# Performance work log

Measured on AMD Instinct MI355X. Metric: run time of the kernel, lower is better.

## Reference

```python
import jax, jax.numpy as jnp
import numpy as np

SEQ, D_IN, D_OUT = 8192, 768, 768

def setup_inputs() -> dict:
    key = jax.random.key(0)
    k1, k2, k3, k4 = jax.random.split(key, 4)
    scale = 1.0 / np.sqrt(D_IN)
    return {
        "x": jax.random.normal(k1, (SEQ, D_IN), dtype=jnp.float32),
        "w_q": jax.random.normal(k2, (D_OUT, D_IN), dtype=jnp.float32) * scale,
        "w_k": jax.random.normal(k3, (D_OUT, D_IN), dtype=jnp.float32) * scale,
        "w_v": jax.random.normal(k4, (D_OUT, D_IN), dtype=jnp.float32) * scale,
    }

def reference(x, w_q, w_k, w_v):
    # torch Linear: y = x @ W.T (no bias since qkv_bias=False)
    q = x @ w_q.T  # [S, D]
    k = x @ w_k.T  # [S, D]
    v = x @ w_v.T  # [S, D]
    scores = (q @ k.T) / jnp.sqrt(jnp.asarray(k.shape[-1], x.dtype))  # [S, S]
    attn = jax.nn.softmax(scores, axis=-1)
    return attn @ v  # [S, D]
```

## Files before the change

### kernel.cpp

```cpp
#include <hip/hip_runtime.h>

#define SEQ 8192
#define DIM 768

typedef __attribute__((ext_vector_type(8))) short s16x8;
typedef __attribute__((ext_vector_type(4))) float f32x4;

__device__ __forceinline__ unsigned short f2bf(float f) {
  union { float f; unsigned u; } v; v.f = f;
  unsigned r = v.u + 0x7FFFu + ((v.u >> 16) & 1u);
  return (unsigned short)(r >> 16);
}

__device__ __forceinline__ float bf2f(unsigned short s) {
  union { unsigned u; float f; } v; v.u = ((unsigned)s) << 16;
  return v.f;
}

__device__ __forceinline__ void gll16(const void* gsrc, void* ldst) {
  __builtin_amdgcn_global_load_lds(
      (__attribute__((address_space(1))) unsigned int*)gsrc,
      (__attribute__((address_space(3))) unsigned int*)ldst, 16, 0, 0);
}

#define XN4 (SEQ * DIM / 4)
#define WN4 (DIM * DIM / 4)

__global__ void cast_all_kernel(const float* __restrict__ x, const float* __restrict__ wq,
                                const float* __restrict__ wk, const float* __restrict__ wv,
                                unsigned short* __restrict__ dx, unsigned short* __restrict__ dq,
                                unsigned short* __restrict__ dk, unsigned short* __restrict__ dv) {
  int i = blockIdx.x * blockDim.x + threadIdx.x;
  const float* s;
  unsigned short* d;
  int off;
  if (i < XN4) {
    s = x; d = dx; off = i;
  } else {
    int j = i - XN4;
    int wi = j / WN4;
    off = j - wi * WN4;
    s = (wi == 0) ? wq : ((wi == 1) ? wk : wv);
    d = (wi == 0) ? dq : ((wi == 1) ? dk : dv);
  }
  float4 v = ((const float4*)s)[off];
  ushort4 r; r.x = f2bf(v.x); r.y = f2bf(v.y); r.z = f2bf(v.z); r.w = f2bf(v.w);
  ((ushort4*)d)[off] = r;
}

__global__ __launch_bounds__(256, 2)
void proj_kernel(const unsigned short* __restrict__ X,
                 const unsigned short* __restrict__ Wq,
                 const unsigned short* __restrict__ Wk,
                 const unsigned short* __restrict__ Wv,
                 unsigned short* __restrict__ Qb,
                 unsigned short* __restrict__ Kb,
                 unsigned short* __restrict__ Vtb) {
  __shared__ __align__(16) char lds[65536];
  const int tid = threadIdx.x;
  const int lane = tid & 63, wv = tid >> 6;
  const int l15 = lane & 15, l4 = lane >> 4;
  const int mt = blockIdx.x, nt = blockIdx.y, z = blockIdx.z;
  const unsigned short* W = (z == 0) ? Wq : ((z == 1) ? Wk : Wv);

  f32x4 acc[4][4];
#pragma unroll
  for (int i = 0; i < 4; ++i)
#pragma unroll
    for (int j = 0; j < 4; ++j) acc[i][j] = f32x4{0.f, 0.f, 0.f, 0.f};

  auto stage = [&](int kk) {
    char* At = lds + (kk & 1) * 32768;
    char* Bt = At + 16384;
    const int d0 = kk * 64;
#pragma unroll
    for (int i = 0; i < 4; ++i) {
      int s = i * 256 + tid;
      int row = s >> 3, c = (s & 7) ^ (row & 7);
      gll16(X + (long)(mt * 128 + row) * DIM + d0 + c * 8, At + i * 4096 + (wv << 10));
      gll16(W + (long)(nt * 128 + row) * DIM + d0 + c * 8, Bt + i * 4096 + (wv << 10));
    }
  };

  stage(0);
#pragma unroll 1
  for (int kk = 0; kk < 12; ++kk) {
    __syncthreads();
    if (kk + 1 < 12) stage(kk + 1);
    const char* At = lds + (kk & 1) * 32768;
    const char* Bt = At + 16384;
#pragma unroll
    for (int ks = 0; ks < 2; ++ks) {
      const int c = ks * 4 + l4;
      s16x8 a[4], b[4];
#pragma unroll
      for (int mi = 0; mi < 4; ++mi) {
        int row = (wv & 1) * 64 + mi * 16 + l15;
        a[mi] = *(const s16x8*)(At + row * 128 + ((c ^ (row & 7)) << 4));
      }
#pragma unroll
      for (int ni = 0; ni < 4; ++ni) {
        int row = (wv >> 1) * 64 + ni * 16 + l15;
        b[ni] = *(const s16x8*)(Bt + row * 128 + ((c ^ (row & 7)) << 4));
      }
#pragma unroll
      for (int mi = 0; mi < 4; ++mi)
#pragma unroll
        for (int ni = 0; ni < 4; ++ni)
          acc[mi][ni] = __builtin_amdgcn_mfma_f32_16x16x32_bf16(a[mi], b[ni], acc[mi][ni], 0, 0, 0);
    }
  }

#pragma unroll
  for (int mi = 0; mi < 4; ++mi)
#pragma unroll
    for (int ni = 0; ni < 4; ++ni) {
      int row0 = mt * 128 + (wv & 1) * 64 + mi * 16 + l4 * 4;
      int col = nt * 128 + (wv >> 1) * 64 + ni * 16 + l15;
      if (z == 2) {
        ushort4 r;
        r.x = f2bf(acc[mi][ni][0]); r.y = f2bf(acc[mi][ni][1]);
        r.z = f2bf(acc[mi][ni][2]); r.w = f2bf(acc[mi][ni][3]);
        *(ushort4*)(Vtb + (long)(row0 >> 5) * (DIM * 32) + col * 32 + (row0 & 31)) = r;
      } else {
        unsigned short* dst = (z == 0) ? Qb : Kb;
#pragma unroll
        for (int g = 0; g < 4; ++g)
          dst[(long)(row0 + g) * DIM + col] = f2bf(acc[mi][ni][g]);
      }
    }
}

#define SCALE_LOG2E 0.05205878f

#define LOADVB(arr, vv)                                                            \
  do {                                                                             \
    const unsigned short* Vb_ = V + (long)(kblk0 + (vv)) * (DIM * 32);             \
    _Pragma("unroll")                                                              \
    for (int j_ = 0; j_ < 6; ++j_)                                                 \
      arr[j_] = *(const s16x8*)(Vb_ + (j_ * 128 + wv * 16 + l15) * 32 + l4 * 8);   \
  } while (0)

#define PVCHUNK(vv, CUR, NXT)                                                      \
  do {                                                                             \
    if ((vv) + 1 < 8) LOADVB(NXT, (vv) + 1);                                       \
    s16x8 pa_[4];                                                                  \
    const int ck_ = (vv) * 4 + l4;                                                 \
    _Pragma("unroll")                                                              \
    for (int rs_ = 0; rs_ < 4; ++rs_) {                                            \
      int row_ = rs_ * 16 + l15;                                                   \
      int pc_ = (ck_ & ~7) | ((ck_ & 7) ^ (row_ & 7));                             \
      pa_[rs_] = *(const s16x8*)(Pl + row_ * 512 + (pc_ << 4));                    \
    }                                                                              \
    __builtin_amdgcn_s_setprio(1);                                                 \
    _Pragma("unroll")                                                              \
    for (int j_ = 0; j_ < 6; ++j_)                                                 \
      _Pragma("unroll")                                                            \
      for (int rs_ = 0; rs_ < 4; ++rs_)                                            \
        acc_o[rs_][j_] =                                                           \
            __builtin_amdgcn_mfma_f32_16x16x32_bf16(pa_[rs_], CUR[j_], acc_o[rs_][j_], 0, 0, 0); \
    __builtin_amdgcn_s_setprio(0);                                                 \
  } while (0)

__global__ __launch_bounds__(512, 2)
void flash_kernel(const unsigned short* __restrict__ Q,
                  const unsigned short* __restrict__ K,
                  const unsigned short* __restrict__ V,
                  unsigned short* __restrict__ partp,
                  float* __restrict__ outf,
                  float* __restrict__ lout,
                  int kv_len, int norm_out) {
  __shared__ __align__(16) char lds[114688];
  char* Pl = lds + 81920;
  float* l_part = (float*)lds;

  const int tid = threadIdx.x;
  const int lane = tid & 63, wv = tid >> 6;
  const int l15 = lane & 15, l4 = lane >> 4;
  const int qtile = blockIdx.x, split = blockIdx.y;
  const long kv0 = (long)split * kv_len;
  const long qrow0 = (long)qtile * 64;
  const int R = wv & 1;
  const int C = wv >> 1;

  f32x4 acc_o[4][6];
  float acc_lp[8];
#pragma unroll
  for (int i = 0; i < 4; ++i)
#pragma unroll
    for (int j = 0; j < 6; ++j) acc_o[i][j] = f32x4{0.f, 0.f, 0.f, 0.f};
#pragma unroll
  for (int i = 0; i < 8; ++i) acc_lp[i] = 0.f;

  const int niter = kv_len >> 8;

  auto stageQK = [&](int r, long kbase) {
    char* Qc = lds + (r & 1) * 40960;
    char* Kc = Qc + 8192;
    const int d0 = r * 64;
    {
      int s = tid;
      int row = s >> 3, c = (s & 7) ^ (row & 7);
      gll16(Q + (qrow0 + row) * DIM + d0 + c * 8, Qc + (wv << 10));
    }
#pragma unroll
    for (int i = 0; i < 4; ++i) {
      int s = i * 512 + tid;
      int row = s >> 3, c = (s & 7) ^ (row & 7);
      gll16(K + (kbase + row) * DIM + d0 + c * 8, Kc + i * 8192 + (wv << 10));
    }
  };

  stageQK(0, kv0);
#pragma unroll 1
  for (int it = 0; it < niter; ++it) {
    const long kb = kv0 + (long)it * 256;
    const long kblk0 = kb >> 5;

    f32x4 acc_s[2][4];
#pragma unroll
    for (int a = 0; a < 2; ++a)
#pragma unroll
      for (int b = 0; b < 4; ++b) acc_s[a][b] = f32x4{0.f, 0.f, 0.f, 0.f};

#pragma unroll 1
    for (int r = 0; r < 12; ++r) {
      __syncthreads();
      if (r + 1 < 12) stageQK(r + 1, kb);
      else if (it + 1 < niter) stageQK(0, kb + 256);
      const char* Qc = lds + (r & 1) * 40960;
      const char* Kc = Qc + 8192;
#pragma unroll
      for (int ks = 0; ks < 2; ++ks) {
        const int c = ks * 4 + l4;
        s16x8 af[2], bk[4];
#pragma unroll
        for (int rt = 0; rt < 2; ++rt) {
          int row = R * 32 + rt * 16 + l15;
          af[rt] = *(const s16x8*)(Qc + row * 128 + ((c ^ (row & 7)) << 4));
        }
#pragma unroll
        for (int ct = 0; ct < 4; ++ct) {
          int kr = C * 64 + ct * 16 + l15;
          bk[ct] = *(const s16x8*)(Kc + kr * 128 + ((c ^ (kr & 7)) << 4));
        }
        __builtin_amdgcn_s_setprio(1);
#pragma unroll
        for (int rt = 0; rt < 2; ++rt)
#pragma unroll
          for (int ct = 0; ct < 4; ++ct)
            acc_s[rt][ct] = __builtin_amdgcn_mfma_f32_16x16x32_bf16(af[rt], bk[ct], acc_s[rt][ct], 0, 0, 0);
        __builtin_amdgcn_s_setprio(0);
      }
    }

    s16x8 vbA[6], vbB[6];
    LOADVB(vbA, 0);

#pragma unroll
    for (int rt = 0; rt < 2; ++rt)
#pragma unroll
      for (int ct = 0; ct < 4; ++ct)
#pragma unroll
        for (int g = 0; g < 4; ++g) {
          float p = exp2f(acc_s[rt][ct][g] * SCALE_LOG2E);
          acc_lp[rt * 4 + g] += p;
          int row = R * 32 + rt * 16 + l4 * 4 + g;
          int col = C * 64 + ct * 16 + l15;
          int off = row * 512 + ((((col >> 3) ^ (row & 7))) << 4) + ((col & 7) << 1);
          *(unsigned short*)(Pl + off) = f2bf(p);
        }
    __syncthreads();

    PVCHUNK(0, vbA, vbB);
    PVCHUNK(1, vbB, vbA);
    PVCHUNK(2, vbA, vbB);
    PVCHUNK(3, vbB, vbA);
    PVCHUNK(4, vbA, vbB);
    PVCHUNK(5, vbB, vbA);
    PVCHUNK(6, vbA, vbB);
    PVCHUNK(7, vbB, vbA);
  }

#pragma unroll
  for (int i = 0; i < 8; ++i) {
    float v = acc_lp[i];
    v += __shfl_xor(v, 1); v += __shfl_xor(v, 2);
    v += __shfl_xor(v, 4); v += __shfl_xor(v, 8);
    acc_lp[i] = v;
  }
  __syncthreads();
  if (l15 == 0) {
#pragma unroll
    for (int rt = 0; rt < 2; ++rt)
#pragma unroll
      for (int g = 0; g < 4; ++g)
        l_part[C * 64 + R * 32 + rt * 16 + l4 * 4 + g] = acc_lp[rt * 4 + g];
  }
  __syncthreads();

  if (!norm_out) {
    if (tid < 64)
      lout[(long)split * SEQ + qrow0 + tid] =
          l_part[tid] + l_part[64 + tid] + l_part[128 + tid] + l_part[192 + tid];
#pragma unroll
    for (int rt = 0; rt < 4; ++rt) {
      int row = rt * 16 + l4 * 4;
#pragma unroll
      for (int j = 0; j < 6; ++j) {
        int cc = j >> 1, t = j & 1;
        int col = (cc * 16 + wv + 8 * t) * 16 + l15;
#pragma unroll
        for (int g = 0; g < 4; ++g)
          partp[(long)split * SEQ * DIM + (qrow0 + row + g) * DIM + col] = f2bf(acc_o[rt][j][g]);
      }
    }
  } else {
    float linv[4][4];
#pragma unroll
    for (int rt = 0; rt < 4; ++rt)
#pragma unroll
      for (int g = 0; g < 4; ++g) {
        int row = rt * 16 + l4 * 4 + g;
        linv[rt][g] = 1.0f / (l_part[row] + l_part[64 + row] + l_part[128 + row] + l_part[192 + row]);
      }
#pragma unroll
    for (int rt = 0; rt < 4; ++rt) {
      int row = rt * 16 + l4 * 4;
#pragma unroll
      for (int j = 0; j < 6; ++j) {
        int cc = j >> 1, t = j & 1;
        int col = (cc * 16 + wv + 8 * t) * 16 + l15;
#pragma unroll
        for (int g = 0; g < 4; ++g)
          outf[(qrow0 + row + g) * DIM + col] = acc_o[rt][j][g] * linv[rt][g];
      }
    }
  }
}

__global__ void combine_kernel(const unsigned short* __restrict__ part,
                               const float* __restrict__ lsum,
                               float* __restrict__ out, int n4) {
  int i = blockIdx.x * blockDim.x + threadIdx.x;
  if (i >= n4) return;
  int row = (i * 4) / DIM;
  ushort4 p0 = ((const ushort4*)part)[i];
  ushort4 p1 = ((const ushort4*)(part + (long)SEQ * DIM))[i];
  float inv = 1.0f / (lsum[row] + lsum[SEQ + row]);
  float4 o;
  o.x = (bf2f(p0.x) + bf2f(p1.x)) * inv;
  o.y = (bf2f(p0.y) + bf2f(p1.y)) * inv;
  o.z = (bf2f(p0.z) + bf2f(p1.z)) * inv;
  o.w = (bf2f(p0.w) + bf2f(p1.w)) * inv;
  ((float4*)out)[i] = o;
}

extern "C" void kernel_launch(void* const* d_in, const int* in_sizes, int n_in,
                              void* d_out, int out_size, void* d_ws, size_t ws_size,
                              hipStream_t stream) {
  const float* x = (const float*)d_in[0];
  const float* wq = (const float*)d_in[1];
  const float* wk = (const float*)d_in[2];
  const float* wv = (const float*)d_in[3];
  float* out = (float*)d_out;
  char* ws = (char*)d_ws;

  const size_t o_xbf = 0;
  const size_t o_wq = o_xbf + (size_t)SEQ * DIM * 2;
  const size_t o_wk = o_wq + (size_t)DIM * DIM * 2;
  const size_t o_wv = o_wk + (size_t)DIM * DIM * 2;
  const size_t o_q = o_wv + (size_t)DIM * DIM * 2;
  const size_t o_k = o_q + (size_t)SEQ * DIM * 2;
  const size_t o_vt = o_k + (size_t)SEQ * DIM * 2;
  const size_t o_part = o_vt + (size_t)SEQ * DIM * 2;
  const size_t o_l = o_part + (size_t)2 * SEQ * DIM * 2;
  const size_t total_g2 = o_l + (size_t)2 * SEQ * 4;

  unsigned short* Xbf = (unsigned short*)(ws + o_xbf);
  unsigned short* Wqb = (unsigned short*)(ws + o_wq);
  unsigned short* Wkb = (unsigned short*)(ws + o_wk);
  unsigned short* Wvb = (unsigned short*)(ws + o_wv);
  unsigned short* Qb = (unsigned short*)(ws + o_q);
  unsigned short* Kb = (unsigned short*)(ws + o_k);
  unsigned short* Vtb = (unsigned short*)(ws + o_vt);
  unsigned short* part = (unsigned short*)(ws + o_part);
  float* lbuf = (float*)(ws + o_l);

  const int G = (ws_size >= total_g2) ? 2 : 1;

  cast_all_kernel<<<7872, 256, 0, stream>>>(x, wq, wk, wv, Xbf, Wqb, Wkb, Wvb);
  proj_kernel<<<dim3(64, 6, 3), 256, 0, stream>>>(Xbf, Wqb, Wkb, Wvb, Qb, Kb, Vtb);
  if (G == 2) {
    flash_kernel<<<dim3(128, 2), 512, 0, stream>>>(Qb, Kb, Vtb, part, nullptr, lbuf, SEQ / 2, 0);
    combine_kernel<<<6144, 256, 0, stream>>>(part, lbuf, out, SEQ * DIM / 4);
  } else {
    flash_kernel<<<dim3(128, 1), 512, 0, stream>>>(Qb, Kb, Vtb, nullptr, out, nullptr, SEQ, 1);
  }
}
```

Measured before the change: 301.4 us.

## Store Q in MFMA-fragment layout and load it directly from global memory

```diff
diff --git a/kernel.cpp b/kernel.cpp
--- a/kernel.cpp
+++ b/kernel.cpp
@@ -122,11 +122,15 @@
         r.x = f2bf(acc[mi][ni][0]); r.y = f2bf(acc[mi][ni][1]);
         r.z = f2bf(acc[mi][ni][2]); r.w = f2bf(acc[mi][ni][3]);
         *(ushort4*)(Vtb + (long)(row0 >> 5) * (DIM * 32) + col * 32 + (row0 & 31)) = r;
+      } else if (z == 0) {
+        const long fb = ((long)(row0 >> 4) * 96 + (col >> 3)) * 128 + (col & 7);
+#pragma unroll
+        for (int g = 0; g < 4; ++g)
+          Qb[fb + (l4 * 4 + g) * 8] = f2bf(acc[mi][ni][g]);
       } else {
-        unsigned short* dst = (z == 0) ? Qb : Kb;
 #pragma unroll
         for (int g = 0; g < 4; ++g)
-          dst[(long)(row0 + g) * DIM + col] = f2bf(acc[mi][ni][g]);
+          Kb[(long)(row0 + g) * DIM + col] = f2bf(acc[mi][ni][g]);
       }
     }
 }
@@ -163,15 +167,15 @@
   } while (0)
 
 __global__ __launch_bounds__(512, 2)
-void flash_kernel(const unsigned short* __restrict__ Q,
+void flash_kernel(const unsigned short* __restrict__ Qf,
                   const unsigned short* __restrict__ K,
                   const unsigned short* __restrict__ V,
                   unsigned short* __restrict__ partp,
                   float* __restrict__ outf,
                   float* __restrict__ lout,
                   int kv_len, int norm_out) {
-  __shared__ __align__(16) char lds[114688];
-  char* Pl = lds + 81920;
+  __shared__ __align__(16) char lds[163840];
+  char* Pl = lds + 131072;
   float* l_part = (float*)lds;
 
   const int tid = threadIdx.x;
@@ -194,24 +198,19 @@
 
   const int niter = kv_len >> 8;
 
-  auto stageQK = [&](int r, long kbase) {
-    char* Qc = lds + (r & 1) * 40960;
-    char* Kc = Qc + 8192;
-    const int d0 = r * 64;
-    {
-      int s = tid;
-      int row = s >> 3, c = (s & 7) ^ (row & 7);
-      gll16(Q + (qrow0 + row) * DIM + d0 + c * 8, Qc + (wv << 10));
-    }
-#pragma unroll
-    for (int i = 0; i < 4; ++i) {
+  auto stageK = [&](int r, long kbase) {
+    char* Kc = lds + (r & 1) * 65536;
+    const int d0 = r * 128;
+#pragma unroll
+    for (int i = 0; i < 8; ++i) {
       int s = i * 512 + tid;
-      int row = s >> 3, c = (s & 7) ^ (row & 7);
+      int row = s >> 4, p = s & 15;
+      int c = p ^ (row & 15);
       gll16(K + (kbase + row) * DIM + d0 + c * 8, Kc + i * 8192 + (wv << 10));
     }
   };
 
-  stageQK(0, kv0);
+  stageK(0, kv0);
 #pragma unroll 1
   for (int it = 0; it < niter; ++it) {
     const long kb = kv0 + (long)it * 256;
@@ -223,33 +222,35 @@
 #pragma unroll
       for (int b = 0; b < 4; ++b) acc_s[a][b] = f32x4{0.f, 0.f, 0.f, 0.f};
 
+    const int tile16q = qtile * 4 + R * 2;
+
 #pragma unroll 1
-    for (int r = 0; r < 12; ++r) {
+    for (int r = 0; r < 6; ++r) {
       __syncthreads();
-      if (r + 1 < 12) stageQK(r + 1, kb);
-      else if (it + 1 < niter) stageQK(0, kb + 256);
-      const char* Qc = lds + (r & 1) * 40960;
-      const char* Kc = Qc + 8192;
-#pragma unroll
-      for (int ks = 0; ks < 2; ++ks) {
-        const int c = ks * 4 + l4;
-        s16x8 af[2], bk[4];
-#pragma unroll
-        for (int rt = 0; rt < 2; ++rt) {
-          int row = R * 32 + rt * 16 + l15;
-          af[rt] = *(const s16x8*)(Qc + row * 128 + ((c ^ (row & 7)) << 4));
-        }
+      if (r + 1 < 6) stageK(r + 1, kb);
+      else if (it + 1 < niter) stageK(0, kb + 256);
+      const char* Kc = lds + (r & 1) * 65536;
+      s16x8 af[2][4];
+#pragma unroll
+      for (int rt = 0; rt < 2; ++rt)
+#pragma unroll
+        for (int ks = 0; ks < 4; ++ks)
+          af[rt][ks] = *(const s16x8*)(Qf +
+              (((long)(tile16q + rt) * 96 + (r * 16 + ks * 4 + l4)) * 16 + l15) * 8);
+#pragma unroll
+      for (int ks = 0; ks < 4; ++ks) {
+        s16x8 bk[4];
 #pragma unroll
         for (int ct = 0; ct < 4; ++ct) {
           int kr = C * 64 + ct * 16 + l15;
-          bk[ct] = *(const s16x8*)(Kc + kr * 128 + ((c ^ (kr & 7)) << 4));
+          bk[ct] = *(const s16x8*)(Kc + kr * 256 + (((ks * 4 + l4) ^ (kr & 15)) << 4));
         }
         __builtin_amdgcn_s_setprio(1);
 #pragma unroll
         for (int rt = 0; rt < 2; ++rt)
 #pragma unroll
           for (int ct = 0; ct < 4; ++ct)
-            acc_s[rt][ct] = __builtin_amdgcn_mfma_f32_16x16x32_bf16(af[rt], bk[ct], acc_s[rt][ct], 0, 0, 0);
+            acc_s[rt][ct] = __builtin_amdgcn_mfma_f32_16x16x32_bf16(af[rt][ks], bk[ct], acc_s[rt][ct], 0, 0, 0);
         __builtin_amdgcn_s_setprio(0);
       }
     }
```

New measurement: 460.2 us. 1.53x slower.
